# Performance work log

Measured on AMD Instinct MI355X. Metric: run time of the kernel, lower is better.

The kernel has to match this reference:

```python
import jax, jax.numpy as jnp
import numpy as np

N_NODES = 100000
N_EDGES = 3200000
F_IN = 54
H = 16


def gcn_conv(x, edge_index, W, b):
    """PyG GCNConv: linear -> add self-loops -> sym-normalized scatter-add -> +bias."""
    n = x.shape[0]
    x = x @ W  # [N, H] transform before propagation (PyG order)
    loop = jnp.arange(n, dtype=edge_index.dtype)
    src = jnp.concatenate([edge_index[0], loop])  # message sources
    dst = jnp.concatenate([edge_index[1], loop])  # aggregation targets
    deg = jax.ops.segment_sum(jnp.ones_like(dst, dtype=x.dtype), dst, num_segments=n)
    dinv = jnp.where(deg > 0, jax.lax.rsqrt(deg), 0.0)
    norm = dinv[src] * dinv[dst]  # D^-1/2 A_hat D^-1/2 edge weights
    msg = x[src] * norm[:, None]  # gather + scale, [E+N, H]
    out = jax.ops.segment_sum(msg, dst, num_segments=n)  # scatter-add
    return out + b


def setup_inputs() -> dict:
    key = jax.random.key(0)
    k = jax.random.split(key, 6)
    x = jax.random.normal(k[0], (N_NODES, F_IN), dtype=jnp.float32)
    edge_index = jax.random.randint(k[1], (2, N_EDGES), 0, N_NODES, dtype=jnp.int64)
    # Glorot-style init for GCNConv weights; bias zeros (PyG default)
    s1 = float(np.sqrt(6.0 / (F_IN + H)))
    s2 = float(np.sqrt(6.0 / (H + H)))
    W1 = jax.random.uniform(k[2], (F_IN, H), dtype=jnp.float32, minval=-s1, maxval=s1)
    b1 = jnp.zeros((H,), dtype=jnp.float32)
    W2 = jax.random.uniform(k[3], (H, H), dtype=jnp.float32, minval=-s2, maxval=s2)
    b2 = jnp.zeros((H,), dtype=jnp.float32)
    return {"x": x, "edge_index": edge_index, "W1": W1, "b1": b1, "W2": W2, "b2": b2}


def reference(x, edge_index, W1, b1, W2, b2):
    h = jax.nn.relu(gcn_conv(x, edge_index, W1, b1))
    # F.dropout(p=0.5, training=self.training) -> identity in eval mode
    h = jax.nn.relu(gcn_conv(h, edge_index, W2, b2))
    return h
```

## Files before the change

kernel.cpp:

```cpp
#include <hip/hip_runtime.h>
#include <hip/hip_fp16.h>

#define HDIM 16
#define FIN 54
#define BSHIFT 7
#define BNODES (1 << BSHIFT)
#define NBMAXB 800
#define NBBMAX 512
#define FBT 1024
#define LST 512
#define FPE 6272
#define PADCOL 6144
#define GPAD 55

__global__ __launch_bounds__(FBT)
void fill_binned_kernel(const int* __restrict__ src, const int* __restrict__ dst,
                        int* __restrict__ lps, unsigned int* __restrict__ binned,
                        int E, int nb, int nbb, int per) {
    __shared__ unsigned int stage[FPE];
    __shared__ int lh[NBMAXB], lcur[NBMAXB];
    __shared__ int ls[FBT];
    int blk = blockIdx.x;
    int s0 = blk * per;
    int s1 = min(E, s0 + per);
    int tot = s1 - s0;
    int t = threadIdx.x;

    for (int b = t; b < nb; b += FBT) lh[b] = 0;
    __syncthreads();
    int idx = s0 + (t << 2);
    for (; idx + 3 < s1; idx += (FBT << 2)) {
        int4 d4 = *(const int4*)&dst[idx];
        atomicAdd(&lh[d4.x >> BSHIFT], 1);
        atomicAdd(&lh[d4.y >> BSHIFT], 1);
        atomicAdd(&lh[d4.z >> BSHIFT], 1);
        atomicAdd(&lh[d4.w >> BSHIFT], 1);
    }
    if (idx < s1) {
        int stop = min(idx + 4, s1);
        for (int e = idx; e < stop; ++e) atomicAdd(&lh[dst[e] >> BSHIFT], 1);
    }
    __syncthreads();
    ls[t] = (t < nb) ? lh[t] : 0;
    __syncthreads();
    for (int d = 1; d < FBT; d <<= 1) {
        int v = (t >= d) ? ls[t - d] : 0;
        __syncthreads();
        ls[t] += v;
        __syncthreads();
    }
    if (t <= nb) {
        int excl = ls[t] - ((t < nb) ? lh[t] : 0);
        if (t < nb) lcur[t] = excl;
        lps[t * nbb + blk] = excl;
    }
    __syncthreads();
    idx = s0 + (t << 2);
    for (; idx + 3 < s1; idx += (FBT << 2)) {
        int4 d4 = *(const int4*)&dst[idx];
        int4 v4 = *(const int4*)&src[idx];
        int p0 = atomicAdd(&lcur[d4.x >> BSHIFT], 1);
        int p1 = atomicAdd(&lcur[d4.y >> BSHIFT], 1);
        int p2 = atomicAdd(&lcur[d4.z >> BSHIFT], 1);
        int p3 = atomicAdd(&lcur[d4.w >> BSHIFT], 1);
        stage[p0] = ((unsigned int)v4.x << BSHIFT) | (unsigned int)(d4.x & (BNODES - 1));
        stage[p1] = ((unsigned int)v4.y << BSHIFT) | (unsigned int)(d4.y & (BNODES - 1));
        stage[p2] = ((unsigned int)v4.z << BSHIFT) | (unsigned int)(d4.z & (BNODES - 1));
        stage[p3] = ((unsigned int)v4.w << BSHIFT) | (unsigned int)(d4.w & (BNODES - 1));
    }
    if (idx < s1) {
        int stop = min(idx + 4, s1);
        for (int e = idx; e < stop; ++e) {
            int d = dst[e];
            int pos = atomicAdd(&lcur[d >> BSHIFT], 1);
            stage[pos] = ((unsigned int)src[e] << BSHIFT) | (unsigned int)(d & (BNODES - 1));
        }
    }
    __syncthreads();
    for (int k = t; k < tot; k += FBT) binned[s0 + k] = stage[k];
}

__global__ __launch_bounds__(LST)
void sort_gemm_kernel(const unsigned int* __restrict__ binned,
                      const int* __restrict__ lps,
                      const float* __restrict__ x, const float* __restrict__ W1,
                      unsigned int* __restrict__ col, int* __restrict__ cs,
                      int* __restrict__ ce, float* __restrict__ dinv,
                      __half* __restrict__ hA,
                      int n, int nb, int nbb, int per) {
    __shared__ int st[NBBMAX], en[NBBMAX];
    __shared__ int hist[BNODES], scn[BNODES], cur[BNODES];
    __shared__ char ubuf[32768];
    unsigned int* stage = (unsigned int*)ubuf;
    float* xl = (float*)ubuf;
    float* Wl = (float*)(ubuf + BNODES * GPAD * 4);

    int b = blockIdx.x;
    int t = threadIdx.x;
    int colbase = b * PADCOL;
    int row0 = b << BSHIFT;
    int nrows = min(BNODES, n - row0);

    for (int blk = t; blk < nbb; blk += LST) {
        st[blk] = lps[b * nbb + blk];
        en[blk] = lps[(b + 1) * nbb + blk];
    }
    if (t < BNODES) hist[t] = 0;
    __syncthreads();

    int g = t >> 3, l = t & 7;
    for (int blk = g; blk < nbb; blk += (LST >> 3)) {
        int base = blk * per;
        int e = en[blk];
        for (int k = st[blk] + l; k < e; k += 8)
            atomicAdd(&hist[binned[base + k] & (BNODES - 1)], 1);
    }
    __syncthreads();
    if (t < BNODES) scn[t] = hist[t];
    __syncthreads();
    for (int d = 1; d < BNODES; d <<= 1) {
        int v = (t < BNODES && t >= d) ? scn[t - d] : 0;
        __syncthreads();
        if (t < BNODES) scn[t] += v;
        __syncthreads();
    }
    float di = 0.0f;
    if (t < BNODES) {
        int excl = scn[t] - hist[t];
        cur[t] = excl;
        int node = row0 + t;
        di = rsqrtf((float)hist[t] + 1.0f);
        if (node < n) {
            cs[node] = colbase + excl;
            ce[node] = colbase + excl + hist[t];
            dinv[node] = di;
        }
    }
    __syncthreads();
    for (int blk = g; blk < nbb; blk += (LST >> 3)) {
        int base = blk * per;
        int e = en[blk];
        for (int k = st[blk] + l; k < e; k += 8) {
            unsigned int p = binned[base + k];
            int pos = atomicAdd(&cur[p & (BNODES - 1)], 1);
            unsigned int sv = p >> BSHIFT;
            if (pos < PADCOL) stage[pos] = sv;
            else col[colbase + pos] = sv;
        }
    }
    __syncthreads();
    int len = scn[BNODES - 1];
    if (len > PADCOL) len = PADCOL;
    for (int k = t; k < len; k += LST) col[colbase + k] = stage[k];
    __syncthreads();
    const float* xb = x + (size_t)row0 * FIN;
    int tot = nrows * FIN;
    for (int i4 = t; i4 < (tot >> 2); i4 += LST) {
        float4 v = ((const float4*)xb)[i4];
        int i = i4 << 2;
        int r = i / FIN;
        int c = i - r * FIN;
#pragma unroll
        for (int u = 0; u < 4; ++u) {
            int cc = c + u, rr = r;
            if (cc >= FIN) { cc -= FIN; ++rr; }
            xl[rr * GPAD + cc] = (&v.x)[u];
        }
    }
    for (int i = (tot & ~3) + t; i < tot; i += LST) {
        int r = i / FIN;
        xl[r * GPAD + (i - r * FIN)] = xb[i];
    }
    for (int k = t; k < FIN * HDIM; k += LST) Wl[k] = W1[k];
    __syncthreads();
    if (t < nrows) {
        const float* xr = &xl[t * GPAD];
        float acc[HDIM];
#pragma unroll
        for (int j = 0; j < HDIM; ++j) acc[j] = 0.0f;
#pragma unroll
        for (int k = 0; k < FIN; ++k) {
            float xv = xr[k];
#pragma unroll
            for (int j = 0; j < HDIM; ++j)
                acc[j] = fmaf(xv, Wl[k * HDIM + j], acc[j]);
        }
        __half2 hh[8];
#pragma unroll
        for (int j = 0; j < 8; ++j)
            hh[j] = __floats2half2_rn(di * acc[2 * j], di * acc[2 * j + 1]);
        uint4* yo = (uint4*)(hA + ((size_t)(row0 + t) << 4));
        yo[0] = *(uint4*)&hh[0];
        yo[1] = *(uint4*)&hh[4];
    }
}

__device__ __forceinline__ float4 ld_h4(const __half* __restrict__ hsh,
                                        unsigned int node, int q) {
    uint2 u = *(const uint2*)(hsh + ((size_t)node << 4) + (q << 2));
    __half2 a = *(__half2*)&u.x;
    __half2 b = *(__half2*)&u.y;
    float2 fa = __half22float2(a);
    float2 fb = __half22float2(b);
    return make_float4(fa.x, fa.y, fb.x, fb.y);
}

template <bool FUSE_W2>
__global__ void gather_kernel(const unsigned int* __restrict__ col,
                              const int* __restrict__ cs, const int* __restrict__ ce,
                              const __half* __restrict__ hsh, const float* __restrict__ dinv,
                              const float* __restrict__ bias, const float* __restrict__ W2,
                              __half* __restrict__ outh, float4* __restrict__ out4, int n) {
    __shared__ float4 W2l[HDIM * 4];
    if constexpr (FUSE_W2) {
        for (int t = threadIdx.x; t < HDIM * 4; t += blockDim.x)
            W2l[t] = ((const float4*)W2)[t];
        __syncthreads();
    }
    int idx = blockIdx.x * blockDim.x + threadIdx.x;
    int i = idx >> 3;
    int sub = idx & 7;
    int q = sub & 3;
    int h = sub >> 2;
    if (i >= n) return;
    int k0 = cs[i], k1 = ce[i];

    float4 acc = (h == 0) ? ld_h4(hsh, (unsigned int)i, q)
                          : make_float4(0.f, 0.f, 0.f, 0.f);
    int k = k0 + h;
    for (; k + 14 < k1; k += 16) {
        unsigned int s[8];
#pragma unroll
        for (int u = 0; u < 8; ++u) s[u] = col[k + 2 * u];
        float4 hv[8];
#pragma unroll
        for (int u = 0; u < 8; ++u) hv[u] = ld_h4(hsh, s[u], q);
#pragma unroll
        for (int u = 0; u < 8; ++u) {
            acc.x += hv[u].x; acc.y += hv[u].y; acc.z += hv[u].z; acc.w += hv[u].w;
        }
    }
    for (; k + 6 < k1; k += 8) {
        unsigned int s[4];
#pragma unroll
        for (int u = 0; u < 4; ++u) s[u] = col[k + 2 * u];
        float4 hv[4];
#pragma unroll
        for (int u = 0; u < 4; ++u) hv[u] = ld_h4(hsh, s[u], q);
#pragma unroll
        for (int u = 0; u < 4; ++u) {
            acc.x += hv[u].x; acc.y += hv[u].y; acc.z += hv[u].z; acc.w += hv[u].w;
        }
    }
    for (; k < k1; k += 2) {
        float4 hv = ld_h4(hsh, col[k], q);
        acc.x += hv.x; acc.y += hv.y; acc.z += hv.z; acc.w += hv.w;
    }
    acc.x += __shfl_xor(acc.x, 4);
    acc.y += __shfl_xor(acc.y, 4);
    acc.z += __shfl_xor(acc.z, 4);
    acc.w += __shfl_xor(acc.w, 4);

    float di = dinv[i];
    float4 b4 = ((const float4*)bias)[q];
    float4 r;
    r.x = fmaxf(fmaf(di, acc.x, b4.x), 0.0f);
    r.y = fmaxf(fmaf(di, acc.y, b4.y), 0.0f);
    r.z = fmaxf(fmaf(di, acc.z, b4.z), 0.0f);
    r.w = fmaxf(fmaf(di, acc.w, b4.w), 0.0f);

    if constexpr (FUSE_W2) {
        int lane = threadIdx.x & 63;
        int base = lane & ~7;
        float4 o = make_float4(0.f, 0.f, 0.f, 0.f);
#pragma unroll
        for (int p = 0; p < 4; ++p) {
            float rx = __shfl(r.x, base + p, 64);
            float ry = __shfl(r.y, base + p, 64);
            float rz = __shfl(r.z, base + p, 64);
            float rw = __shfl(r.w, base + p, 64);
            float4 w0 = W2l[(p * 4 + 0) * 4 + q];
            float4 w1 = W2l[(p * 4 + 1) * 4 + q];
            float4 w2 = W2l[(p * 4 + 2) * 4 + q];
            float4 w3 = W2l[(p * 4 + 3) * 4 + q];
            o.x = fmaf(rx, w0.x, fmaf(ry, w1.x, fmaf(rz, w2.x, fmaf(rw, w3.x, o.x))));
            o.y = fmaf(rx, w0.y, fmaf(ry, w1.y, fmaf(rz, w2.y, fmaf(rw, w3.y, o.y))));
            o.z = fmaf(rx, w0.z, fmaf(ry, w1.z, fmaf(rz, w2.z, fmaf(rw, w3.z, o.z))));
            o.w = fmaf(rx, w0.w, fmaf(ry, w1.w, fmaf(rz, w2.w, fmaf(rw, w3.w, o.w))));
        }
        if (h == 0) {
            __half2 o01 = __floats2half2_rn(di * o.x, di * o.y);
            __half2 o23 = __floats2half2_rn(di * o.z, di * o.w);
            uint2 pk;
            pk.x = *(unsigned int*)&o01;
            pk.y = *(unsigned int*)&o23;
            *(uint2*)(outh + ((size_t)i << 4) + (q << 2)) = pk;
        }
    } else {
        if (h == 0) out4[(size_t)i * 4 + q] = r;
    }
}

extern "C" void kernel_launch(void* const* d_in, const int* in_sizes, int n_in,
                              void* d_out, int out_size, void* d_ws, size_t ws_size,
                              hipStream_t stream) {
    const float* x  = (const float*)d_in[0];
    const int*   ei = (const int*)d_in[1];
    const float* W1 = (const float*)d_in[2];
    const float* b1 = (const float*)d_in[3];
    const float* W2 = (const float*)d_in[4];
    const float* b2 = (const float*)d_in[5];
    float* out = (float*)d_out;

    const int E = in_sizes[1] / 2;
    const int n = in_sizes[0] / FIN;
    const int* src = ei;
    const int* dst = ei + E;
    const int nb = (n + BNODES - 1) >> BSHIFT;

    int nbb = (E + 6251) / 6252;
    if (nbb > NBBMAX) nbb = NBBMAX;
    int per = (((E + nbb - 1) / nbb) + 3) & ~3;

    char* w = (char*)d_ws;
    auto take = [&](size_t bytes) { char* p = w; w += (bytes + 255) & ~(size_t)255; return p; };
    float* dinv = (float*)take((size_t)n * 4);
    int*   lps  = (int*)take((size_t)(nb + 1) * nbb * 4);
    int*   cs   = (int*)take((size_t)n * 4);
    int*   ce   = (int*)take((size_t)n * 4);
    unsigned int* binned = (unsigned int*)take((size_t)nbb * per * 4);
    __half* hA  = (__half*)take((size_t)n * HDIM * 2);
    __half* hB  = (__half*)take((size_t)n * HDIM * 2);
    unsigned int* col = (unsigned int*)take((size_t)nb * PADCOL * 4);

    const int B = 256;

    fill_binned_kernel<<<nbb, FBT, 0, stream>>>(src, dst, lps, binned, E, nb, nbb, per);
    sort_gemm_kernel<<<nb, LST, 0, stream>>>(binned, lps, x, W1, col, cs, ce, dinv,
                                             hA, n, nb, nbb, per);

    gather_kernel<true><<<(n * 8 + B - 1) / B, B, 0, stream>>>(
        col, cs, ce, hA, dinv, b1, W2, hB, nullptr, n);

    gather_kernel<false><<<(n * 8 + B - 1) / B, B, 0, stream>>>(
        col, cs, ce, hB, dinv, b2, nullptr, nullptr, (float4*)out, n);
}
```

Before: 96.25 us.

## Cache binned edges in LDS during histogram pass and halve fill block count

```diff
diff --git a/kernel.cpp b/kernel.cpp
--- a/kernel.cpp
+++ b/kernel.cpp
@@ -9,7 +9,8 @@
 #define NBBMAX 512
 #define FBT 1024
 #define LST 512
-#define FPE 6272
+#define FPE 12544
+#define EBE 6272
 #define PADCOL 6144
 #define GPAD 55
 
@@ -88,9 +89,12 @@
                       int* __restrict__ ce, float* __restrict__ dinv,
                       __half* __restrict__ hA,
                       int n, int nb, int nbb, int per) {
-    __shared__ int st[NBBMAX], en[NBBMAX];
+    __shared__ int st[NBBMAX], en[NBBMAX], co[NBBMAX];
     __shared__ int hist[BNODES], scn[BNODES], cur[BNODES];
+    __shared__ unsigned int ebuf[EBE];
+    __shared__ int lensh;
     __shared__ char ubuf[32768];
+    int* ls = (int*)ubuf;
     unsigned int* stage = (unsigned int*)ubuf;
     float* xl = (float*)ubuf;
     float* Wl = (float*)(ubuf + BNODES * GPAD * 4);
@@ -107,13 +111,28 @@
     }
     if (t < BNODES) hist[t] = 0;
     __syncthreads();
-
-    int g = t >> 3, l = t & 7;
-    for (int blk = g; blk < nbb; blk += (LST >> 3)) {
+    ls[t] = (t < nbb) ? (en[t] - st[t]) : 0;
+    __syncthreads();
+    for (int d = 1; d < LST; d <<= 1) {
+        int v = (t >= d) ? ls[t - d] : 0;
+        __syncthreads();
+        ls[t] += v;
+        __syncthreads();
+    }
+    if (t < nbb) co[t] = ls[t] - (en[t] - st[t]);
+    if (t == 0) lensh = ls[nbb - 1];
+    __syncthreads();
+
+    int g = t >> 4, l = t & 15;
+    for (int blk = g; blk < nbb; blk += (LST >> 4)) {
         int base = blk * per;
-        int e = en[blk];
-        for (int k = st[blk] + l; k < e; k += 8)
-            atomicAdd(&hist[binned[base + k] & (BNODES - 1)], 1);
+        int s = st[blk], e = en[blk], c = co[blk] - s;
+        for (int k = s + l; k < e; k += 16) {
+            unsigned int p = binned[base + k];
+            int pos = c + k;
+            if (pos < EBE) ebuf[pos] = p;
+            atomicAdd(&hist[p & (BNODES - 1)], 1);
+        }
     }
     __syncthreads();
     if (t < BNODES) scn[t] = hist[t];
@@ -137,21 +156,34 @@
         }
     }
     __syncthreads();
-    for (int blk = g; blk < nbb; blk += (LST >> 3)) {
-        int base = blk * per;
-        int e = en[blk];
-        for (int k = st[blk] + l; k < e; k += 8) {
-            unsigned int p = binned[base + k];
-            int pos = atomicAdd(&cur[p & (BNODES - 1)], 1);
-            unsigned int sv = p >> BSHIFT;
-            if (pos < PADCOL) stage[pos] = sv;
-            else col[colbase + pos] = sv;
-        }
-    }
-    __syncthreads();
-    int len = scn[BNODES - 1];
-    if (len > PADCOL) len = PADCOL;
-    for (int k = t; k < len; k += LST) col[colbase + k] = stage[k];
+    int len = lensh;
+    int lim = min(len, EBE);
+    for (int k = t; k < lim; k += LST) {
+        unsigned int p = ebuf[k];
+        int pos = atomicAdd(&cur[p & (BNODES - 1)], 1);
+        unsigned int sv = p >> BSHIFT;
+        if (pos < PADCOL) stage[pos] = sv;
+        else col[colbase + pos] = sv;
+    }
+    if (len > EBE) {
+        for (int blk = g; blk < nbb; blk += (LST >> 4)) {
+            int base = blk * per;
+            int s = st[blk], e = en[blk], c = co[blk] - s;
+            for (int k = s + l; k < e; k += 16) {
+                if (c + k >= EBE) {
+                    unsigned int p = binned[base + k];
+                    int pos = atomicAdd(&cur[p & (BNODES - 1)], 1);
+                    unsigned int sv = p >> BSHIFT;
+                    if (pos < PADCOL) stage[pos] = sv;
+                    else col[colbase + pos] = sv;
+                }
+            }
+        }
+    }
+    __syncthreads();
+    int flen = scn[BNODES - 1];
+    if (flen > PADCOL) flen = PADCOL;
+    for (int k = t; k < flen; k += LST) col[colbase + k] = stage[k];
     __syncthreads();
     const float* xb = x + (size_t)row0 * FIN;
     int tot = nrows * FIN;
@@ -318,7 +350,7 @@
     const int* dst = ei + E;
     const int nb = (n + BNODES - 1) >> BSHIFT;
 
-    int nbb = (E + 6251) / 6252;
+    int nbb = (E + 12499) / 12500;
     if (nbb > NBBMAX) nbb = NBBMAX;
     int per = (((E + nbb - 1) / nbb) + 3) & ~3;
 
```

Result: no change. 97.27 us (+1.1%).
